# Performance work log

Measured on AMD Instinct MI355X. Metric: run time of the kernel, lower is better.

The kernel has to match this reference:

```python
import jax, jax.numpy as jnp
import numpy as np

K = 32          # kneighbors
HEADS = 4       # Anchor_selfattention head_num
EPS = 1e-5      # BatchNorm eps


def bn(x, gamma, beta):
    # training-mode BatchNorm1d on channel-last tensor [B, M, C]:
    # stats over batch+spatial dims per channel, biased variance (torch behavior)
    m = jnp.mean(x, axis=(0, 1), keepdims=True)
    v = jnp.var(x, axis=(0, 1), keepdims=True)
    return gamma * (x - m) * jax.lax.rsqrt(v + EPS) + beta


def setup_inputs() -> dict:
    B, NA, NP, C, NRAW = 32, 4, 16384, 256, 32768
    key = jax.random.key(0)
    ks = jax.random.split(key, 12)
    s = 0.02
    return {
        "a_points": jax.random.normal(ks[0], (B, NA, 3), jnp.float32),
        "sa_x": jax.random.normal(ks[1], (B, NP, C), jnp.float32),
        "sa_xyz": jax.random.normal(ks[2], (B, NP, 3), jnp.float32),
        "xyz_raw": jax.random.normal(ks[3], (B, NRAW, 3), jnp.float32),
        # global_layer: Conv1d(3->C, bias=False) + BN(C)
        "g_W": jax.random.normal(ks[4], (C, 3), jnp.float32) * s,
        "g_gamma": jnp.ones((C,), jnp.float32),
        "g_beta": jnp.zeros((C,), jnp.float32),
        # attention: to_qkv Linear(C -> 3C, bias=False)
        "qkv_W": jax.random.normal(ks[5], (3 * C, C), jnp.float32) * s,
        # pos_embedding: Conv1d(3->C) + BN(C)
        "pos_W": jax.random.normal(ks[6], (C, 3), jnp.float32) * s,
        "pos_b": jnp.zeros((C,), jnp.float32),
        "pos_gamma": jnp.ones((C,), jnp.float32),
        "pos_beta": jnp.zeros((C,), jnp.float32),
        # res: Conv1d(C->C) + BN(C)
        "res_W": jax.random.normal(ks[7], (C, C), jnp.float32) * s,
        "res_b": jnp.zeros((C,), jnp.float32),
        "res_gamma": jnp.ones((C,), jnp.float32),
        "res_beta": jnp.zeros((C,), jnp.float32),
        # prob_head: Conv1d(2C -> 9, bias=False) + BN(9)
        "prob_W": jax.random.normal(ks[8], (9, 2 * C), jnp.float32) * s,
        "prob_gamma": jnp.ones((9,), jnp.float32),
        "prob_beta": jnp.zeros((9,), jnp.float32),
    }


def reference(a_points, sa_x, sa_xyz, xyz_raw,
              g_W, g_gamma, g_beta,
              qkv_W,
              pos_W, pos_b, pos_gamma, pos_beta,
              res_W, res_b, res_gamma, res_beta,
              prob_W, prob_gamma, prob_beta):
    B, NA, _ = a_points.shape
    C = sa_x.shape[-1]
    hd = C // HEADS

    # ---- knn_point: squared distances anchor->points, smallest-K indices ----
    # dist[b, a, n] = |a_points[b,a] - sa_xyz[b,n]|^2
    d = (-2.0 * jnp.einsum("bac,bnc->ban", a_points, sa_xyz)
         + jnp.sum(a_points ** 2, -1)[:, :, None]
         + jnp.sum(sa_xyz ** 2, -1)[:, None, :])
    _, idx = jax.lax.top_k(-d, K)                      # [B, NA, K]

    # ---- index_points gather + max-pool over neighbors ----
    local = jnp.take_along_axis(sa_x[:, None, :, :], idx[..., None], axis=2)  # [B,NA,K,C]
    local_feat = jnp.max(local, axis=2)                # [B, NA, C]

    # ---- Anchor self-attention ----
    gc = jnp.mean(a_points, axis=1, keepdims=True)
    rel = a_points - gc                                # [B, NA, 3]
    pos = bn(rel @ pos_W.T + pos_b, pos_gamma, pos_beta)   # [B, NA, C]

    qkv = local_feat @ qkv_W.T                         # [B, NA, 3C]
    q, k, v = jnp.split(qkv, 3, axis=-1)
    q, k, v = q + pos, k + pos, v + pos
    q = q.reshape(B, NA, HEADS, hd)
    k = k.reshape(B, NA, HEADS, hd)
    v = v.reshape(B, NA, HEADS, hd)
    attn = jnp.einsum("bmhd,bnhd->bhmn", q, k) / np.sqrt(hd).astype(np.float32)
    attn = jax.nn.softmax(attn, axis=-1)
    av = jnp.einsum("bhmn,bnhd->bmhd", attn, v).reshape(B, NA, C)
    res = bn(av @ res_W.T + res_b, res_gamma, res_beta)

    local_feat = local_feat + res                      # [B, NA, C]

    # ---- global branch ----
    gfeat = bn(a_points @ g_W.T, g_gamma, g_beta)      # [B, NA, C]
    gmax = jnp.max(gfeat, axis=1, keepdims=True)       # [B, 1, C]
    feat = jnp.concatenate(
        [local_feat, jnp.broadcast_to(gmax, (B, NA, C))], axis=-1)  # [B, NA, 2C]

    prob = bn(feat @ prob_W.T, prob_gamma, prob_beta)  # [B, NA, 9]
    return prob
```

## Files before the change

kernel.cpp:

```cpp
#include <hip/hip_runtime.h>
#include <math.h>

#define NPTS 16384
#define NB   32
#define NA   4
#define NC   256
#define KNN  32
#define NROW 128
#define CAP  2048

#define OFF_QKV     32768
#define OFF_RESLIN  131072
#define OFF_PROBLIN 163840

__global__ __launch_bounds__(512) void knn_kernel(
    const float* __restrict__ a_points, const float* __restrict__ sa_xyz,
    const float* __restrict__ sa_x, const float* __restrict__ qkv_W,
    float* __restrict__ lf, float* __restrict__ qkv)
{
  const int blk = blockIdx.x;
  const int b   = blk >> 2;
  const int t   = threadIdx.x;

  __shared__ float s_T;
  __shared__ int   s_m;
  __shared__ uint2 s_cand[CAP];
  __shared__ int   s_top[KNN];
  __shared__ float s_lf2[2][NC];
  __shared__ float lf_s[NC];
  float* smin = (float*)s_cand;

  const float ax = a_points[blk*3 + 0];
  const float ay = a_points[blk*3 + 1];
  const float az = a_points[blk*3 + 2];
  const float* __restrict__ xyz = sa_xyz + (size_t)b * NPTS * 3;

  float d[32];
#pragma unroll
  for (int j = 0; j < 32; ++j) {
    const int n = t + 512*j;
    const float dx = xyz[n*3+0] - ax;
    const float dy = xyz[n*3+1] - ay;
    const float dz = xyz[n*3+2] - az;
    d[j] = dx*dx + dy*dy + dz*dz;
  }
  float mn = d[0];
#pragma unroll
  for (int j = 1; j < 32; ++j) mn = fminf(mn, d[j]);
  if (t == 0) s_m = 0;
  smin[t] = mn;
  __syncthreads();

  if (t < 64) {
    unsigned v[8];
#pragma unroll
    for (int q = 0; q < 8; ++q) v[q] = __float_as_uint(smin[t + 64*q]);
    unsigned lo = 0u, hi = 0x7f7fffffu;
    while (lo < hi) {
      const unsigned mid = lo + ((hi - lo) >> 1);
      int cnt = 0;
#pragma unroll
      for (int q = 0; q < 8; ++q) cnt += (int)__popcll(__ballot(v[q] <= mid));
      if (cnt >= KNN) hi = mid; else lo = mid + 1;
    }
    if (t == 0) s_T = __uint_as_float(lo);
  }
  __syncthreads();
  const float T = s_T;

#pragma unroll
  for (int j = 0; j < 32; ++j) {
    if (d[j] <= T) {
      const int pos = atomicAdd(&s_m, 1);
      if (pos < CAP) s_cand[pos] = make_uint2(__float_as_uint(d[j]), (unsigned)(t + 512*j));
    }
  }
  __syncthreads();
  const int m = (s_m < CAP) ? s_m : CAP;

  for (int c2 = t; c2 < m; c2 += 512) {
    const uint2 me = s_cand[c2];
    int rank = 0;
    for (int j = 0; j < m; ++j) {
      const uint2 o = s_cand[j];
      rank += (o.x < me.x) || (o.x == me.x && o.y < me.y);
    }
    if (rank < KNN) s_top[rank] = (int)me.y;
  }
  __syncthreads();

  {
    const int c = t & 255, h = t >> 8;
    const float* __restrict__ xb = sa_x + (size_t)b * NPTS * NC;
    float acc = -3.0e38f;
    for (int r = h*16; r < h*16 + 16; ++r)
      acc = fmaxf(acc, xb[(size_t)s_top[r] * NC + c]);
    s_lf2[h][c] = acc;
  }
  __syncthreads();
  if (t < NC) {
    const float v = fmaxf(s_lf2[0][t], s_lf2[1][t]);
    lf_s[t] = v;
    lf[(size_t)blk * NC + t] = v;
  }
  __syncthreads();

  {
    const float* __restrict__ w1 = qkv_W + (size_t)t * NC;
    float a1 = 0.f;
    for (int c = 0; c < NC; c += 4) {
      const float4 l4 = *(const float4*)&lf_s[c];
      const float4 w4 = *(const float4*)(w1 + c);
      a1 = fmaf(l4.x,w4.x,a1); a1 = fmaf(l4.y,w4.y,a1); a1 = fmaf(l4.z,w4.z,a1); a1 = fmaf(l4.w,w4.w,a1);
    }
    qkv[(size_t)blk*768 + t] = a1;
    if (t < 256) {
      const float* __restrict__ w2 = qkv_W + (size_t)(512 + t) * NC;
      float a2 = 0.f;
      for (int c = 0; c < NC; c += 4) {
        const float4 l4 = *(const float4*)&lf_s[c];
        const float4 w4 = *(const float4*)(w2 + c);
        a2 = fmaf(l4.x,w4.x,a2); a2 = fmaf(l4.y,w4.y,a2); a2 = fmaf(l4.z,w4.z,a2); a2 = fmaf(l4.w,w4.w,a2);
      }
      qkv[(size_t)blk*768 + 512 + t] = a2;
    }
  }
}

__global__ __launch_bounds__(256) void attn_kernel(
    const float* __restrict__ a_points, const float* __restrict__ qkv,
    const float* __restrict__ pos_W, const float* __restrict__ pos_b,
    const float* __restrict__ pos_gamma, const float* __restrict__ pos_beta,
    const float* __restrict__ res_W, const float* __restrict__ res_b,
    float* __restrict__ res_lin)
{
  const int b = blockIdx.x;
  const int t = threadIdx.x;
  __shared__ float apts[NROW * 3];
  __shared__ float av_s[NA][NC];
  for (int i = t; i < NROW*3; i += 256) apts[i] = a_points[i];
  __syncthreads();

  const int c = t;
  const float pw0 = pos_W[c*3+0], pw1 = pos_W[c*3+1], pw2 = pos_W[c*3+2];
  const float pbb = pos_b[c];
  float psum = 0.f, pss = 0.f;
  float posv[NA];
#pragma unroll
  for (int a = 0; a < NA; ++a) posv[a] = 0.f;
  for (int b2 = 0; b2 < NB; ++b2) {
    float gx=0.f, gy=0.f, gz=0.f;
#pragma unroll
    for (int a = 0; a < NA; ++a) {
      gx += apts[(b2*NA+a)*3+0];
      gy += apts[(b2*NA+a)*3+1];
      gz += apts[(b2*NA+a)*3+2];
    }
    gx *= 0.25f; gy *= 0.25f; gz *= 0.25f;
#pragma unroll
    for (int a = 0; a < NA; ++a) {
      const float v = (apts[(b2*NA+a)*3+0]-gx)*pw0
                    + (apts[(b2*NA+a)*3+1]-gy)*pw1
                    + (apts[(b2*NA+a)*3+2]-gz)*pw2 + pbb;
      psum += v; pss += v*v;
      if (b2 == b) posv[a] = v;
    }
  }
  const float pmean = psum * (1.0f/NROW);
  const float pvar  = pss * (1.0f/NROW) - pmean*pmean;
  const float prstd = 1.0f / sqrtf(pvar + 1e-5f);
  const float pga = pos_gamma[c], pbe = pos_beta[c];

  float q[NA], k[NA], vv[NA];
#pragma unroll
  for (int a = 0; a < NA; ++a) {
    const int row = b*NA + a;
    const float p = pga * (posv[a] - pmean) * prstd + pbe;
    q[a]  = qkv[(size_t)row*768 +       c] + p;
    k[a]  = qkv[(size_t)row*768 + 256 + c] + p;
    vv[a] = qkv[(size_t)row*768 + 512 + c] + p;
  }
  float s[NA][NA];
#pragma unroll
  for (int m = 0; m < NA; ++m) {
#pragma unroll
    for (int n = 0; n < NA; ++n) {
      float p = q[m]*k[n];
#pragma unroll
      for (int off = 1; off < 64; off <<= 1) p += __shfl_xor(p, off);
      s[m][n] = p * 0.125f;
    }
  }
#pragma unroll
  for (int m = 0; m < NA; ++m) {
    const float mx = fmaxf(fmaxf(s[m][0], s[m][1]), fmaxf(s[m][2], s[m][3]));
    const float e0 = expf(s[m][0]-mx), e1 = expf(s[m][1]-mx);
    const float e2 = expf(s[m][2]-mx), e3 = expf(s[m][3]-mx);
    const float inv = 1.0f / (e0+e1+e2+e3);
    av_s[m][c] = (e0*vv[0] + e1*vv[1] + e2*vv[2] + e3*vv[3]) * inv;
  }
  __syncthreads();

  const float* __restrict__ wrow = res_W + (size_t)c * NC;
  float r0=0.f, r1=0.f, r2=0.f, r3=0.f;
  for (int cc = 0; cc < NC; cc += 4) {
    const float4 w4 = *(const float4*)(wrow + cc);
    const float4 v0 = *(const float4*)&av_s[0][cc];
    const float4 v1 = *(const float4*)&av_s[1][cc];
    const float4 v2 = *(const float4*)&av_s[2][cc];
    const float4 v3 = *(const float4*)&av_s[3][cc];
    r0 = fmaf(v0.x,w4.x,r0); r0 = fmaf(v0.y,w4.y,r0); r0 = fmaf(v0.z,w4.z,r0); r0 = fmaf(v0.w,w4.w,r0);
    r1 = fmaf(v1.x,w4.x,r1); r1 = fmaf(v1.y,w4.y,r1); r1 = fmaf(v1.z,w4.z,r1); r1 = fmaf(v1.w,w4.w,r1);
    r2 = fmaf(v2.x,w4.x,r2); r2 = fmaf(v2.y,w4.y,r2); r2 = fmaf(v2.z,w4.z,r2); r2 = fmaf(v2.w,w4.w,r2);
    r3 = fmaf(v3.x,w4.x,r3); r3 = fmaf(v3.y,w4.y,r3); r3 = fmaf(v3.z,w4.z,r3); r3 = fmaf(v3.w,w4.w,r3);
  }
  const float bias = res_b[c];
  res_lin[(size_t)(b*NA+0)*NC + c] = r0 + bias;
  res_lin[(size_t)(b*NA+1)*NC + c] = r1 + bias;
  res_lin[(size_t)(b*NA+2)*NC + c] = r2 + bias;
  res_lin[(size_t)(b*NA+3)*NC + c] = r3 + bias;
}

__global__ __launch_bounds__(256) void final_kernel(
    const float* __restrict__ a_points,
    const float* __restrict__ lf, const float* __restrict__ res_lin,
    const float* __restrict__ res_gamma, const float* __restrict__ res_beta,
    const float* __restrict__ g_W, const float* __restrict__ g_gamma, const float* __restrict__ g_beta,
    const float* __restrict__ prob_W,
    float* __restrict__ prob_lin)
{
  const int b = blockIdx.x;
  const int t = threadIdx.x;
  __shared__ float apts[NROW * 3];
  __shared__ float feat_s[NA][2 * NC];
  for (int i = t; i < NROW*3; i += 256) apts[i] = a_points[i];
  __syncthreads();

  const int c = t;
  float rsum = 0.f, rss = 0.f;
  for (int row = 0; row < NROW; ++row) {
    const float v = res_lin[(size_t)row*NC + c];
    rsum += v; rss += v*v;
  }
  const float rmean = rsum * (1.0f/NROW);
  const float rvar  = rss * (1.0f/NROW) - rmean*rmean;
  const float rrstd = 1.0f / sqrtf(rvar + 1e-5f);
  const float rg = res_gamma[c], rb = res_beta[c];

  const float gw0 = g_W[c*3+0], gw1 = g_W[c*3+1], gw2 = g_W[c*3+2];
  float gsum = 0.f, gss = 0.f;
  for (int row = 0; row < NROW; ++row) {
    const float v = apts[row*3+0]*gw0 + apts[row*3+1]*gw1 + apts[row*3+2]*gw2;
    gsum += v; gss += v*v;
  }
  const float gmean = gsum * (1.0f/NROW);
  const float gvar  = gss * (1.0f/NROW) - gmean*gmean;
  const float grstd = 1.0f / sqrtf(gvar + 1e-5f);
  const float gg = g_gamma[c], gb = g_beta[c];

  float gm = -3.0e38f;
#pragma unroll
  for (int a = 0; a < NA; ++a) {
    const int row = b*NA + a;
    const float gv = apts[row*3+0]*gw0 + apts[row*3+1]*gw1 + apts[row*3+2]*gw2;
    gm = fmaxf(gm, gg * (gv - gmean) * grstd + gb);
  }
#pragma unroll
  for (int a = 0; a < NA; ++a) {
    const int row = b*NA + a;
    const float resv = rg * (res_lin[(size_t)row*NC + c] - rmean) * rrstd + rb;
    feat_s[a][c]      = lf[(size_t)row*NC + c] + resv;
    feat_s[a][NC + c] = gm;
  }
  __syncthreads();

  const int m = t >> 6, lane = t & 63;
  for (int j = 0; j < 9; ++j) {
    float p = 0.f;
#pragma unroll
    for (int k2 = 0; k2 < 8; ++k2) {
      const int cc = lane + 64*k2;
      p = fmaf(feat_s[m][cc], prob_W[j*2*NC + cc], p);
    }
#pragma unroll
    for (int off = 1; off < 64; off <<= 1) p += __shfl_xor(p, off);
    if (lane == 0) prob_lin[(b*NA+m)*9 + j] = p;
  }
}

__global__ __launch_bounds__(256) void out_kernel(
    const float* __restrict__ prob_lin,
    const float* __restrict__ prob_gamma, const float* __restrict__ prob_beta,
    float* __restrict__ out)
{
  const int t = threadIdx.x;
  __shared__ float pmn[9], prs[9];
  if (t < 9) {
    float s = 0.f, ss = 0.f;
    for (int i = 0; i < NROW; ++i) { const float v = prob_lin[i*9+t]; s += v; ss += v*v; }
    const float m  = s * (1.0f/NROW);
    const float va = ss * (1.0f/NROW) - m*m;
    pmn[t] = m; prs[t] = 1.0f / sqrtf(va + 1e-5f);
  }
  __syncthreads();
  for (int i = t; i < NROW*9; i += 256) {
    const int j = i % 9;
    out[i] = prob_gamma[j] * (prob_lin[i] - pmn[j]) * prs[j] + prob_beta[j];
  }
}

extern "C" void kernel_launch(void* const* d_in, const int* in_sizes, int n_in,
                              void* d_out, int out_size, void* d_ws, size_t ws_size,
                              hipStream_t stream) {
  const float* a_points  = (const float*)d_in[0];
  const float* sa_x      = (const float*)d_in[1];
  const float* sa_xyz    = (const float*)d_in[2];
  const float* g_W       = (const float*)d_in[4];
  const float* g_gamma   = (const float*)d_in[5];
  const float* g_beta    = (const float*)d_in[6];
  const float* qkv_W     = (const float*)d_in[7];
  const float* pos_W     = (const float*)d_in[8];
  const float* pos_b     = (const float*)d_in[9];
  const float* pos_gamma = (const float*)d_in[10];
  const float* pos_beta  = (const float*)d_in[11];
  const float* res_W     = (const float*)d_in[12];
  const float* res_b     = (const float*)d_in[13];
  const float* res_gamma = (const float*)d_in[14];
  const float* res_beta  = (const float*)d_in[15];
  const float* prob_W    = (const float*)d_in[16];
  const float* prob_gamma= (const float*)d_in[17];
  const float* prob_beta = (const float*)d_in[18];
  float* ws  = (float*)d_ws;
  float* out = (float*)d_out;

  knn_kernel<<<NROW, 512, 0, stream>>>(a_points, sa_xyz, sa_x, qkv_W,
      ws, ws + OFF_QKV);
  attn_kernel<<<NB, 256, 0, stream>>>(a_points, ws + OFF_QKV,
      pos_W, pos_b, pos_gamma, pos_beta, res_W, res_b, ws + OFF_RESLIN);
  final_kernel<<<NB, 256, 0, stream>>>(a_points, ws, ws + OFF_RESLIN,
      res_gamma, res_beta, g_W, g_gamma, g_beta, prob_W, ws + OFF_PROBLIN);
  out_kernel<<<1, 256, 0, stream>>>(ws + OFF_PROBLIN, prob_gamma, prob_beta, out);
}
```

Before: 70.84 us.

## Split KNN across point halves, separate gather and batched QKV kernels

The KNN search now runs over two halves of the point cloud per anchor (256 blocks instead of 128). Each half writes its top-32 candidates, and a new gather kernel merges the 64 candidates and max-pools the features. The QKV projection moves into a separate tiled kernel that reuses each weight row across 4 rows, and the pos/global BN statistics are computed once instead of per block. This raises parallelism and removes redundant work, at the cost of two extra kernel launches and more workspace round-trips through global memory.

```diff
diff --git a/kernel.cpp b/kernel.cpp
--- a/kernel.cpp
+++ b/kernel.cpp
@@ -2,42 +2,47 @@
 #include <math.h>
 
 #define NPTS 16384
+#define HALF 8192
 #define NB   32
 #define NA   4
 #define NC   256
 #define KNN  32
 #define NROW 128
-#define CAP  2048
-
+#define CAP  1024
+
+#define OFF_LF      0
 #define OFF_QKV     32768
 #define OFF_RESLIN  131072
-#define OFF_PROBLIN 163840
-
-__global__ __launch_bounds__(512) void knn_kernel(
+#define OFF_POSLIN  163840
+#define OFF_POSST   196608
+#define OFF_GLIN    197120
+#define OFF_GST     229888
+#define OFF_PROBLIN 230400
+#define OFF_CAND    231552
+
+__global__ __launch_bounds__(512) void knn_part_kernel(
     const float* __restrict__ a_points, const float* __restrict__ sa_xyz,
-    const float* __restrict__ sa_x, const float* __restrict__ qkv_W,
-    float* __restrict__ lf, float* __restrict__ qkv)
-{
-  const int blk = blockIdx.x;
-  const int b   = blk >> 2;
-  const int t   = threadIdx.x;
+    uint2* __restrict__ cand)
+{
+  const int blk  = blockIdx.x;
+  const int row  = blk >> 1;
+  const int half = blk & 1;
+  const int b    = row >> 2;
+  const int t    = threadIdx.x;
 
   __shared__ float s_T;
   __shared__ int   s_m;
   __shared__ uint2 s_cand[CAP];
-  __shared__ int   s_top[KNN];
-  __shared__ float s_lf2[2][NC];
-  __shared__ float lf_s[NC];
   float* smin = (float*)s_cand;
 
-  const float ax = a_points[blk*3 + 0];
-  const float ay = a_points[blk*3 + 1];
-  const float az = a_points[blk*3 + 2];
-  const float* __restrict__ xyz = sa_xyz + (size_t)b * NPTS * 3;
-
-  float d[32];
-#pragma unroll
-  for (int j = 0; j < 32; ++j) {
+  const float ax = a_points[row*3 + 0];
+  const float ay = a_points[row*3 + 1];
+  const float az = a_points[row*3 + 2];
+  const float* __restrict__ xyz = sa_xyz + (size_t)b * NPTS * 3 + (size_t)half * HALF * 3;
+
+  float d[16];
+#pragma unroll
+  for (int j = 0; j < 16; ++j) {
     const int n = t + 512*j;
     const float dx = xyz[n*3+0] - ax;
     const float dy = xyz[n*3+1] - ay;
@@ -46,7 +51,7 @@
   }
   float mn = d[0];
 #pragma unroll
-  for (int j = 1; j < 32; ++j) mn = fminf(mn, d[j]);
+  for (int j = 1; j < 16; ++j) mn = fminf(mn, d[j]);
   if (t == 0) s_m = 0;
   smin[t] = mn;
   __syncthreads();
@@ -69,10 +74,11 @@
   const float T = s_T;
 
 #pragma unroll
-  for (int j = 0; j < 32; ++j) {
+  for (int j = 0; j < 16; ++j) {
     if (d[j] <= T) {
       const int pos = atomicAdd(&s_m, 1);
-      if (pos < CAP) s_cand[pos] = make_uint2(__float_as_uint(d[j]), (unsigned)(t + 512*j));
+      if (pos < CAP) s_cand[pos] = make_uint2(__float_as_uint(d[j]),
+                                              (unsigned)(half*HALF + t + 512*j));
     }
   }
   __syncthreads();
@@ -85,89 +91,131 @@
       const uint2 o = s_cand[j];
       rank += (o.x < me.x) || (o.x == me.x && o.y < me.y);
     }
+    if (rank < KNN) cand[(size_t)blk*KNN + rank] = me;
+  }
+}
+
+__global__ __launch_bounds__(256) void gather_kernel(
+    const uint2* __restrict__ cand, const float* __restrict__ sa_x,
+    float* __restrict__ lf)
+{
+  const int row = blockIdx.x;
+  const int b   = row >> 2;
+  const int t   = threadIdx.x;
+  __shared__ uint2 s64[64];
+  __shared__ int   s_top[KNN];
+  if (t < 64) s64[t] = cand[(size_t)row*64 + t];
+  __syncthreads();
+  if (t < 64) {
+    const uint2 me = s64[t];
+    int rank = 0;
+#pragma unroll
+    for (int j = 0; j < 64; ++j) {
+      const uint2 o = s64[j];
+      rank += (o.x < me.x) || (o.x == me.x && o.y < me.y);
+    }
     if (rank < KNN) s_top[rank] = (int)me.y;
   }
   __syncthreads();
 
-  {
-    const int c = t & 255, h = t >> 8;
-    const float* __restrict__ xb = sa_x + (size_t)b * NPTS * NC;
-    float acc = -3.0e38f;
-    for (int r = h*16; r < h*16 + 16; ++r)
-      acc = fmaxf(acc, xb[(size_t)s_top[r] * NC + c]);
-    s_lf2[h][c] = acc;
-  }
-  __syncthreads();
-  if (t < NC) {
-    const float v = fmaxf(s_lf2[0][t], s_lf2[1][t]);
-    lf_s[t] = v;
-    lf[(size_t)blk * NC + t] = v;
-  }
-  __syncthreads();
-
-  {
-    const float* __restrict__ w1 = qkv_W + (size_t)t * NC;
-    float a1 = 0.f;
+  const float* __restrict__ xb = sa_x + (size_t)b * NPTS * NC;
+  float acc = -3.0e38f;
+#pragma unroll
+  for (int r = 0; r < KNN; ++r)
+    acc = fmaxf(acc, xb[(size_t)s_top[r] * NC + t]);
+  lf[(size_t)row * NC + t] = acc;
+}
+
+__global__ __launch_bounds__(256) void lin1_kernel(
+    const float* __restrict__ lf, const float* __restrict__ qkv_W,
+    const float* __restrict__ a_points,
+    const float* __restrict__ pos_W, const float* __restrict__ pos_b,
+    const float* __restrict__ g_W,
+    float* __restrict__ qkv, float* __restrict__ pos_lin, float* __restrict__ pos_stats,
+    float* __restrict__ g_lin, float* __restrict__ g_stats)
+{
+  const int blk = blockIdx.x;
+  if (blk < 96) {
+    const int r0 = (blk / 12) * 16;
+    const int o0 = (blk % 12) * 64;
+    const int ot = threadIdx.x & 63;
+    const int rt = threadIdx.x >> 6;
+    const int o  = o0 + ot;
+    const float* __restrict__ wrow = qkv_W + (size_t)o * NC;
+    const float* __restrict__ l0p  = lf + (size_t)(r0 + rt*4) * NC;
+    float acc0 = 0.f, acc1 = 0.f, acc2 = 0.f, acc3 = 0.f;
     for (int c = 0; c < NC; c += 4) {
-      const float4 l4 = *(const float4*)&lf_s[c];
-      const float4 w4 = *(const float4*)(w1 + c);
-      a1 = fmaf(l4.x,w4.x,a1); a1 = fmaf(l4.y,w4.y,a1); a1 = fmaf(l4.z,w4.z,a1); a1 = fmaf(l4.w,w4.w,a1);
-    }
-    qkv[(size_t)blk*768 + t] = a1;
-    if (t < 256) {
-      const float* __restrict__ w2 = qkv_W + (size_t)(512 + t) * NC;
-      float a2 = 0.f;
-      for (int c = 0; c < NC; c += 4) {
-        const float4 l4 = *(const float4*)&lf_s[c];
-        const float4 w4 = *(const float4*)(w2 + c);
-        a2 = fmaf(l4.x,w4.x,a2); a2 = fmaf(l4.y,w4.y,a2); a2 = fmaf(l4.z,w4.z,a2); a2 = fmaf(l4.w,w4.w,a2);
+      const float4 w4 = *(const float4*)(wrow + c);
+      const float4 l0 = *(const float4*)(l0p + c);
+      const float4 l1 = *(const float4*)(l0p + NC + c);
+      const float4 l2 = *(const float4*)(l0p + 2*NC + c);
+      const float4 l3 = *(const float4*)(l0p + 3*NC + c);
+      acc0 = fmaf(l0.x,w4.x,acc0); acc0 = fmaf(l0.y,w4.y,acc0); acc0 = fmaf(l0.z,w4.z,acc0); acc0 = fmaf(l0.w,w4.w,acc0);
+      acc1 = fmaf(l1.x,w4.x,acc1); acc1 = fmaf(l1.y,w4.y,acc1); acc1 = fmaf(l1.z,w4.z,acc1); acc1 = fmaf(l1.w,w4.w,acc1);
+      acc2 = fmaf(l2.x,w4.x,acc2); acc2 = fmaf(l2.y,w4.y,acc2); acc2 = fmaf(l2.z,w4.z,acc2); acc2 = fmaf(l2.w,w4.w,acc2);
+      acc3 = fmaf(l3.x,w4.x,acc3); acc3 = fmaf(l3.y,w4.y,acc3); acc3 = fmaf(l3.z,w4.z,acc3); acc3 = fmaf(l3.w,w4.w,acc3);
+    }
+    const int r = r0 + rt*4;
+    qkv[(size_t)(r+0)*768 + o] = acc0;
+    qkv[(size_t)(r+1)*768 + o] = acc1;
+    qkv[(size_t)(r+2)*768 + o] = acc2;
+    qkv[(size_t)(r+3)*768 + o] = acc3;
+  } else if (blk == 96) {
+    __shared__ float apts[NROW*3];
+    for (int i = threadIdx.x; i < NROW*3; i += 256) apts[i] = a_points[i];
+    __syncthreads();
+    const int c = threadIdx.x;
+    const float w0 = pos_W[c*3+0], w1 = pos_W[c*3+1], w2 = pos_W[c*3+2];
+    const float bb = pos_b[c];
+    float sum = 0.f, sumsq = 0.f;
+    for (int b = 0; b < NB; ++b) {
+      float gx=0.f, gy=0.f, gz=0.f;
+#pragma unroll
+      for (int a = 0; a < NA; ++a) {
+        gx += apts[(b*NA+a)*3+0];
+        gy += apts[(b*NA+a)*3+1];
+        gz += apts[(b*NA+a)*3+2];
       }
-      qkv[(size_t)blk*768 + 512 + t] = a2;
-    }
+      gx *= 0.25f; gy *= 0.25f; gz *= 0.25f;
+#pragma unroll
+      for (int a = 0; a < NA; ++a) {
+        const float v = (apts[(b*NA+a)*3+0]-gx)*w0
+                      + (apts[(b*NA+a)*3+1]-gy)*w1
+                      + (apts[(b*NA+a)*3+2]-gz)*w2 + bb;
+        pos_lin[(b*NA+a)*NC + c] = v;
+        sum += v; sumsq += v*v;
+      }
+    }
+    pos_stats[c] = sum; pos_stats[NC + c] = sumsq;
+  } else {
+    __shared__ float apts[NROW*3];
+    for (int i = threadIdx.x; i < NROW*3; i += 256) apts[i] = a_points[i];
+    __syncthreads();
+    const int c = threadIdx.x;
+    const float w0 = g_W[c*3+0], w1 = g_W[c*3+1], w2 = g_W[c*3+2];
+    float sum = 0.f, sumsq = 0.f;
+    for (int r = 0; r < NROW; ++r) {
+      const float v = apts[r*3+0]*w0 + apts[r*3+1]*w1 + apts[r*3+2]*w2;
+      g_lin[r*NC + c] = v;
+      sum += v; sumsq += v*v;
+    }
+    g_stats[c] = sum; g_stats[NC + c] = sumsq;
   }
 }
 
 __global__ __launch_bounds__(256) void attn_kernel(
-    const float* __restrict__ a_points, const float* __restrict__ qkv,
-    const float* __restrict__ pos_W, const float* __restrict__ pos_b,
+    const float* __restrict__ qkv, const float* __restrict__ pos_lin,
+    const float* __restrict__ pos_stats,
     const float* __restrict__ pos_gamma, const float* __restrict__ pos_beta,
     const float* __restrict__ res_W, const float* __restrict__ res_b,
     float* __restrict__ res_lin)
 {
   const int b = blockIdx.x;
   const int t = threadIdx.x;
-  __shared__ float apts[NROW * 3];
   __shared__ float av_s[NA][NC];
-  for (int i = t; i < NROW*3; i += 256) apts[i] = a_points[i];
-  __syncthreads();
-
   const int c = t;
-  const float pw0 = pos_W[c*3+0], pw1 = pos_W[c*3+1], pw2 = pos_W[c*3+2];
-  const float pbb = pos_b[c];
-  float psum = 0.f, pss = 0.f;
-  float posv[NA];
-#pragma unroll
-  for (int a = 0; a < NA; ++a) posv[a] = 0.f;
-  for (int b2 = 0; b2 < NB; ++b2) {
-    float gx=0.f, gy=0.f, gz=0.f;
-#pragma unroll
-    for (int a = 0; a < NA; ++a) {
-      gx += apts[(b2*NA+a)*3+0];
-      gy += apts[(b2*NA+a)*3+1];
-      gz += apts[(b2*NA+a)*3+2];
-    }
-    gx *= 0.25f; gy *= 0.25f; gz *= 0.25f;
-#pragma unroll
-    for (int a = 0; a < NA; ++a) {
-      const float v = (apts[(b2*NA+a)*3+0]-gx)*pw0
-                    + (apts[(b2*NA+a)*3+1]-gy)*pw1
-                    + (apts[(b2*NA+a)*3+2]-gz)*pw2 + pbb;
-      psum += v; pss += v*v;
-      if (b2 == b) posv[a] = v;
-    }
-  }
-  const float pmean = psum * (1.0f/NROW);
-  const float pvar  = pss * (1.0f/NROW) - pmean*pmean;
+  const float pmean = pos_stats[c] * (1.0f/NROW);
+  const float pvar  = pos_stats[NC + c] * (1.0f/NROW) - pmean*pmean;
   const float prstd = 1.0f / sqrtf(pvar + 1e-5f);
   const float pga = pos_gamma[c], pbe = pos_beta[c];
 
@@ -175,7 +223,7 @@
 #pragma unroll
   for (int a = 0; a < NA; ++a) {
     const int row = b*NA + a;
-    const float p = pga * (posv[a] - pmean) * prstd + pbe;
+    const float p = pga * (pos_lin[(size_t)row*NC + c] - pmean) * prstd + pbe;
     q[a]  = qkv[(size_t)row*768 +       c] + p;
     k[a]  = qkv[(size_t)row*768 + 256 + c] + p;
     vv[a] = qkv[(size_t)row*768 + 512 + c] + p;
@@ -222,20 +270,16 @@
 }
 
 __global__ __launch_bounds__(256) void final_kernel(
-    const float* __restrict__ a_points,
     const float* __restrict__ lf, const float* __restrict__ res_lin,
     const float* __restrict__ res_gamma, const float* __restrict__ res_beta,
-    const float* __restrict__ g_W, const float* __restrict__ g_gamma, const float* __restrict__ g_beta,
+    const float* __restrict__ g_lin, const float* __restrict__ g_stats,
+    const float* __restrict__ g_gamma, const float* __restrict__ g_beta,
     const float* __restrict__ prob_W,
     float* __restrict__ prob_lin)
 {
   const int b = blockIdx.x;
   const int t = threadIdx.x;
-  __shared__ float apts[NROW * 3];
   __shared__ float feat_s[NA][2 * NC];
-  for (int i = t; i < NROW*3; i += 256) apts[i] = a_points[i];
-  __syncthreads();
-
   const int c = t;
   float rsum = 0.f, rss = 0.f;
   for (int row = 0; row < NROW; ++row) {
@@ -247,14 +291,8 @@
   const float rrstd = 1.0f / sqrtf(rvar + 1e-5f);
   const float rg = res_gamma[c], rb = res_beta[c];
 
-  const float gw0 = g_W[c*3+0], gw1 = g_W[c*3+1], gw2 = g_W[c*3+2];
-  float gsum = 0.f, gss = 0.f;
-  for (int row = 0; row < NROW; ++row) {
-    const float v = apts[row*3+0]*gw0 + apts[row*3+1]*gw1 + apts[row*3+2]*gw2;
-    gsum += v; gss += v*v;
-  }
-  const float gmean = gsum * (1.0f/NROW);
-  const float gvar  = gss * (1.0f/NROW) - gmean*gmean;
+  const float gmean = g_stats[c] * (1.0f/NROW);
+  const float gvar  = g_stats[NC+c] * (1.0f/NROW) - gmean*gmean;
   const float grstd = 1.0f / sqrtf(gvar + 1e-5f);
   const float gg = g_gamma[c], gb = g_beta[c];
 
@@ -262,8 +300,7 @@
 #pragma unroll
   for (int a = 0; a < NA; ++a) {
     const int row = b*NA + a;
-    const float gv = apts[row*3+0]*gw0 + apts[row*3+1]*gw1 + apts[row*3+2]*gw2;
-    gm = fmaxf(gm, gg * (gv - gmean) * grstd + gb);
+    gm = fmaxf(gm, gg * (g_lin[(size_t)row*NC + c] - gmean) * grstd + gb);
   }
 #pragma unroll
   for (int a = 0; a < NA; ++a) {
@@ -333,11 +370,14 @@
   float* ws  = (float*)d_ws;
   float* out = (float*)d_out;
 
-  knn_kernel<<<NROW, 512, 0, stream>>>(a_points, sa_xyz, sa_x, qkv_W,
-      ws, ws + OFF_QKV);
-  attn_kernel<<<NB, 256, 0, stream>>>(a_points, ws + OFF_QKV,
-      pos_W, pos_b, pos_gamma, pos_beta, res_W, res_b, ws + OFF_RESLIN);
-  final_kernel<<<NB, 256, 0, stream>>>(a_points, ws, ws + OFF_RESLIN,
-      res_gamma, res_beta, g_W, g_gamma, g_beta, prob_W, ws + OFF_PROBLIN);
+  knn_part_kernel<<<256, 512, 0, stream>>>(a_points, sa_xyz, (uint2*)(ws + OFF_CAND));
+  gather_kernel<<<NROW, 256, 0, stream>>>((const uint2*)(ws + OFF_CAND), sa_x, ws + OFF_LF);
+  lin1_kernel<<<98, 256, 0, stream>>>(ws + OFF_LF, qkv_W, a_points, pos_W, pos_b, g_W,
+      ws + OFF_QKV, ws + OFF_POSLIN, ws + OFF_POSST, ws + OFF_GLIN, ws + OFF_GST);
+  attn_kernel<<<NB, 256, 0, stream>>>(ws + OFF_QKV, ws + OFF_POSLIN, ws + OFF_POSST,
+      pos_gamma, pos_beta, res_W, res_b, ws + OFF_RESLIN);
+  final_kernel<<<NB, 256, 0, stream>>>(ws + OFF_LF, ws + OFF_RESLIN,
+      res_gamma, res_beta, ws + OFF_GLIN, ws + OFF_GST, g_gamma, g_beta, prob_W,
+      ws + OFF_PROBLIN);
   out_kernel<<<1, 256, 0, stream>>>(ws + OFF_PROBLIN, prob_gamma, prob_beta, out);
 }
```

Result: faster. 63.80 us (-9.9%).
